# Optimization experiments

Hardware: AMD Instinct MI355X
Metric: run time of the kernel (lower is better)

The kernel has to match this reference:

```python
import jax, jax.numpy as jnp
import numpy as np

B, T, N, M = 128, 128, 32, 128  # batch, window(input_len), driving_series, hidden_size


def _lstm_cell(x_t, h, c, Wih, Whh, bih, bhh):
    # PyTorch gate order: i, f, g, o
    g = x_t @ Wih.T + bih + h @ Whh.T + bhh
    i, f, gg, o = jnp.split(g, 4, axis=-1)
    c = jax.nn.sigmoid(f) * c + jax.nn.sigmoid(i) * jnp.tanh(gg)
    h = jax.nn.sigmoid(o) * jnp.tanh(c)
    return h, c


def _lstm_seq(x, Wih, Whh, bih, bhh):
    # x: [B,T,n] -> outputs [B,T,m], zero init state
    Bc = x.shape[0]
    m = Whh.shape[1]
    def step(carry, x_t):
        h, c = carry
        h, c = _lstm_cell(x_t, h, c, Wih, Whh, bih, bhh)
        return (h, c), h
    h0 = jnp.zeros((Bc, m), x.dtype)
    (_, _), ys = jax.lax.scan(step, (h0, h0), jnp.swapaxes(x, 0, 1))
    return jnp.swapaxes(ys, 0, 1)


def _forward(x, Wih0, Whh0, bih0, bhh0, We, Ue, Ve,
             Wg, bg, Wa, ba,
             Wih1, Whh1, bih1, bhh1, Wih2, Whh2, bih2, bhh2):
    Bc, Tc, n = x.shape
    m = Whh0.shape[1]
    ux = jnp.einsum('btn,mn->btm', x, Ue)  # Ue(x), constant across steps

    def step(carry, x_t):
        h, c = carry
        hs = jnp.concatenate([h, c], axis=-1)              # [B,2m]
        e = jnp.tanh(ux + (hs @ We.T)[:, None, :]) @ Ve[0]  # [B,T]
        a = jax.nn.softmax(e, axis=1)
        ia_t = jnp.einsum('bt,btn->bn', a, x)              # attended input at step t
        h, c = _lstm_cell(x_t, h, c, Wih0, Whh0, bih0, bhh0)
        return (h, c), ia_t

    h0 = jnp.zeros((Bc, m), x.dtype)
    (_, _), ia = jax.lax.scan(step, (h0, h0), jnp.swapaxes(x, 0, 1))
    input_attention = jnp.swapaxes(ia, 0, 1)               # [B,T,n]

    # self (spatial) attention, fully vectorized over t
    g = jnp.tanh(jnp.einsum('btn,mn->btm', x, Wg) + bg)
    a = jax.nn.sigmoid(jnp.einsum('btm,nm->btn', g, Wa) + ba)
    self_attention = a * x                                  # [B,T,n]

    out1 = _lstm_seq(input_attention, Wih1, Whh1, bih1, bhh1)
    out2 = _lstm_seq(self_attention, Wih2, Whh2, bih2, bhh2)
    return jnp.concatenate([out1, out2], axis=-1)           # [B,T,2m]


def setup_inputs() -> dict:
    key = jax.random.key(0)
    ks = jax.random.split(key, 20)
    stdv = 1.0 / np.sqrt(M)
    u = lambda k, shp: jax.random.uniform(k, shp, jnp.float32, -stdv, stdv)
    inp = {
        'x': jax.random.normal(ks[0], (B, T, N), jnp.float32),
        'Wih0': u(ks[1], (4 * M, N)), 'Whh0': u(ks[2], (4 * M, M)),
        'bih0': u(ks[3], (4 * M,)), 'bhh0': u(ks[4], (4 * M,)),
        'We': u(ks[5], (M, 2 * M)), 'Ue': u(ks[6], (M, N)), 'Ve': u(ks[7], (1, M)),
        'Wg': u(ks[8], (M, N)), 'bg': u(ks[9], (M,)),
        'Wa': u(ks[10], (N, M)), 'ba': u(ks[11], (N,)),
        'Wih1': u(ks[12], (4 * M, N)), 'Whh1': u(ks[13], (4 * M, M)),
        'bih1': u(ks[14], (4 * M,)), 'bhh1': u(ks[15], (4 * M,)),
        'Wih2': u(ks[16], (4 * M, N)), 'Whh2': u(ks[17], (4 * M, M)),
        'bih2': u(ks[18], (4 * M,)), 'bhh2': u(ks[19], (4 * M,)),
    }
    return inp


def reference(x, Wih0, Whh0, bih0, bhh0, We, Ue, Ve, Wg, bg, Wa, ba,
              Wih1, Whh1, bih1, bhh1, Wih2, Whh2, bih2, bhh2):
    return _forward(x, Wih0, Whh0, bih0, bhh0, We, Ue, Ve, Wg, bg, Wa, ba,
                    Wih1, Whh1, bih1, bhh1, Wih2, Whh2, bih2, bhh2)
```

## Files before the change

### kernel.cpp

```cpp
#include <hip/hip_runtime.h>

#define DI __device__ __forceinline__

DI float fsig(float v)  { return 1.0f / (1.0f + __expf(-v)); }
DI float ftanh(float v) { return 1.0f - 2.0f / (__expf(2.0f * v) + 1.0f); }

template <int MODE>
DI void lstm_scan(const float* __restrict__ xin,
                  const float* __restrict__ Wih,
                  const float* __restrict__ Whh,
                  const float* __restrict__ bih,
                  const float* __restrict__ bhh,
                  float* __restrict__ rec,
                  float* __restrict__ outp,
                  float* lds)
{
    const int tid = threadIdx.x;
    float* xl  = lds;
    float* h   = lds + 4096;
    float* c   = lds + 4224;
    float* act = lds + 4352;

    for (int i = tid; i < 4096; i += 512) xl[i] = xin[i];
    if (tid < 128) { h[tid] = 0.f; c[tid] = 0.f; }

    float4 wi[8], wh[32];
    {
        const float4* p = (const float4*)(Wih + tid * 32);
        #pragma unroll
        for (int i = 0; i < 8; ++i) wi[i] = p[i];
        const float4* q2 = (const float4*)(Whh + tid * 128);
        #pragma unroll
        for (int i = 0; i < 32; ++i) wh[i] = q2[i];
    }
    const float bias = bih[tid] + bhh[tid];
    const int gate = tid >> 7;
    __syncthreads();

    for (int t = 0; t < 128; ++t) {
        if (MODE == 0) {
            if (tid < 256) rec[t * 256 + tid] = (tid < 128) ? h[tid] : c[tid - 128];
        }
        float acc = bias;
        const float4* x4 = (const float4*)(xl + t * 32);
        #pragma unroll
        for (int i = 0; i < 8; ++i) {
            float4 v = x4[i];
            acc += wi[i].x * v.x + wi[i].y * v.y + wi[i].z * v.z + wi[i].w * v.w;
        }
        const float4* h4 = (const float4*)h;
        #pragma unroll
        for (int i = 0; i < 32; ++i) {
            float4 v = h4[i];
            acc += wh[i].x * v.x + wh[i].y * v.y + wh[i].z * v.z + wh[i].w * v.w;
        }
        float a = (gate == 2) ? ftanh(acc) : fsig(acc);
        act[tid] = a;
        __syncthreads();
        if (tid < 128) {
            float iv = act[tid], fv = act[128 + tid], gv = act[256 + tid], ov = act[384 + tid];
            float cn = fv * c[tid] + iv * gv;
            float hn = ov * ftanh(cn);
            c[tid] = cn; h[tid] = hn;
            if (MODE == 1) outp[t * 256 + tid] = hn;
        }
        __syncthreads();
    }
}

DI void selfatt_body(const float* __restrict__ x, const float* __restrict__ Wg,
                     const float* __restrict__ bg, const float* __restrict__ Wa,
                     const float* __restrict__ ba, float* __restrict__ sa,
                     int b, float* s)
{
    float* xl  = s;
    float* Wgl = s + 4224;
    float* WaT = s + 8448;
    float* bgl = s + 12672;
    float* bal = s + 12800;
    float* gl  = s + 12832;
    float* pp  = s + 13344;

    const int tid = threadIdx.x;
    for (int i = tid; i < 4096; i += 512) {
        int r = i >> 5, n = i & 31;
        xl[r * 33 + n]  = x[b * 4096 + i];
        Wgl[r * 33 + n] = Wg[i];
        WaT[(i & 127) * 33 + (i >> 7)] = Wa[i];
    }
    if (tid < 128) bgl[tid] = bg[tid];
    else if (tid < 160) bal[tid - 128] = ba[tid - 128];
    __syncthreads();

    const int tl = tid >> 7;
    for (int it = 0; it < 32; ++it) {
        {   const int m = tid & 127;
            const int t = it * 4 + tl;
            float acc = bgl[m];
            #pragma unroll
            for (int n = 0; n < 32; ++n) acc += xl[t * 33 + n] * Wgl[m * 33 + n];
            gl[tl * 128 + m] = ftanh(acc);
        }
        __syncthreads();
        {   const int n = tid & 31, c = (tid >> 5) & 3;
            float acc = 0.f;
            #pragma unroll
            for (int j = 0; j < 32; ++j) {
                int m = c * 32 + j;
                acc += gl[tl * 128 + m] * WaT[m * 33 + n];
            }
            pp[(tl * 4 + c) * 32 + n] = acc;
        }
        __syncthreads();
        if (tid < 128) {
            const int tl2 = tid >> 5, n = tid & 31;
            const int t = it * 4 + tl2;
            float sv = pp[(tl2 * 4 + 0) * 32 + n] + pp[(tl2 * 4 + 1) * 32 + n]
                     + pp[(tl2 * 4 + 2) * 32 + n] + pp[(tl2 * 4 + 3) * 32 + n] + bal[n];
            sa[b * 4096 + t * 32 + n] = fsig(sv) * xl[t * 33 + n];
        }
        __syncthreads();
    }
}

__global__ __launch_bounds__(512)
void kA_lstm0_sa(const float* __restrict__ x,
                 const float* __restrict__ Wih0, const float* __restrict__ Whh0,
                 const float* __restrict__ bih0, const float* __restrict__ bhh0,
                 const float* __restrict__ Wg, const float* __restrict__ bg,
                 const float* __restrict__ Wa, const float* __restrict__ ba,
                 float* __restrict__ rec, float* __restrict__ sa)
{
    __shared__ float smem[13856];
    const int blk = blockIdx.x;
    if (blk < 128) {
        lstm_scan<0>(x + blk * 4096, Wih0, Whh0, bih0, bhh0,
                     rec + blk * 32768, nullptr, smem);
    } else {
        selfatt_body(x, Wg, bg, Wa, ba, sa, blk - 128, smem);
    }
}

__global__ __launch_bounds__(512)
void kC_lstm12(const float* __restrict__ ia, const float* __restrict__ sa,
               const float* __restrict__ Wih1, const float* __restrict__ Whh1,
               const float* __restrict__ bih1, const float* __restrict__ bhh1,
               const float* __restrict__ Wih2, const float* __restrict__ Whh2,
               const float* __restrict__ bih2, const float* __restrict__ bhh2,
               float* __restrict__ out)
{
    __shared__ float smem[4864];
    const int blk = blockIdx.x;
    if (blk < 128) {
        lstm_scan<1>(ia + blk * 4096, Wih1, Whh1, bih1, bhh1,
                     nullptr, out + blk * 32768, smem);
    } else {
        const int b = blk - 128;
        lstm_scan<1>(sa + b * 4096, Wih2, Whh2, bih2, bhh2,
                     nullptr, out + b * 32768 + 128, smem);
    }
}

__global__ __launch_bounds__(512, 4)
void kB_attn(const float* __restrict__ x,
             const float* __restrict__ Ue,
             const float* __restrict__ We,
             const float* __restrict__ Ve,
             const float* __restrict__ rec,
             float* __restrict__ ia)
{
    __shared__ float xl[4608];
    __shared__ float wl[4608];
    __shared__ float ubuf[4608];
    __shared__ float ev[128];
    __shared__ float av[128];
    __shared__ float iap[576];
    __shared__ float wred[2];
    __shared__ float wsum[2];

    const int tid = threadIdx.x;
    const int b  = blockIdx.x >> 2;
    const int tc = blockIdx.x & 3;
    const int ta = tid >> 2;
    const int q  = tid & 3;

    float4 wer[16];
    {
        const float4* p = (const float4*)(We + tid * 64);
        #pragma unroll
        for (int i = 0; i < 16; ++i) wer[i] = p[i];
    }
    for (int i = tid; i < 4096; i += 512)
        xl[(i >> 5) * 36 + (i & 31)] = x[b * 4096 + i];

    const long rbase = (long)b * 32768 + (long)tc * 32 * 256;
    for (int h2 = 0; h2 < 2; ++h2) {
        __syncthreads();
        #pragma unroll
        for (int s = 0; s < 8; ++s) {
            int f = tid + 512 * s;
            int tl = f >> 8, k = f & 255;
            ubuf[tl * 272 + (k >> 6) * 68 + (k & 63)] =
                rec[rbase + (h2 * 16 + tl) * 256 + k];
        }
        __syncthreads();
        for (int tl = 0; tl < 16; ++tl) {
            const float4* hp = (const float4*)(ubuf + tl * 272 + q * 68);
            float acc = 0.f;
            #pragma unroll
            for (int i = 0; i < 16; ++i) {
                float4 v = hp[i];
                acc += wer[i].x * v.x + wer[i].y * v.y + wer[i].z * v.z + wer[i].w * v.w;
            }
            acc += __shfl_xor(acc, 1);
            acc += __shfl_xor(acc, 2);
            if (q == 0)
                wl[(h2 * 16 + tl) * 144 + (ta & 3) * 36 + (ta >> 2)] = 2.0f * acc;
        }
    }
    __syncthreads();

    for (int i = tid; i < 4096; i += 512)
        ubuf[(i >> 5) * 36 + (i & 31)] = Ue[i];
    __syncthreads();

    float uxr[32];
    {
        float xr[32];
        const float4* xp = (const float4*)(xl + ta * 36);
        #pragma unroll
        for (int i = 0; i < 8; ++i) {
            float4 v = xp[i];
            xr[4*i] = v.x; xr[4*i+1] = v.y; xr[4*i+2] = v.z; xr[4*i+3] = v.w;
        }
        #pragma unroll
        for (int j = 0; j < 32; ++j) {
            const float4* up = (const float4*)(ubuf + (4 * j + q) * 36);
            float acc = 0.f;
            #pragma unroll
            for (int i = 0; i < 8; ++i) {
                float4 v = up[i];
                acc += xr[4*i] * v.x + xr[4*i+1] * v.y + xr[4*i+2] * v.z + xr[4*i+3] * v.w;
            }
            uxr[j] = 2.0f * acc;
        }
    }

    float ver[32];
    #pragma unroll
    for (int j = 0; j < 32; ++j) ver[j] = Ve[4 * j + q];
    float VeTot;
    {
        float vs = 0.f;
        #pragma unroll
        for (int j = 0; j < 32; ++j) vs += ver[j];
        vs += __shfl_xor(vs, 1);
        vs += __shfl_xor(vs, 2);
        VeTot = vs;
    }

    for (int tl = 0; tl < 32; ++tl) {
        const int t = tc * 32 + tl;
        float acc2 = 0.f;
        const float4* wr = (const float4*)(wl + tl * 144 + q * 36);
        #pragma unroll
        for (int j4 = 0; j4 < 8; ++j4) {
            float4 w4 = wr[j4];
            {   float zs = uxr[4*j4+0] + w4.x;
                acc2 += ver[4*j4+0] * __fdividef(2.0f, __expf(zs) + 1.0f); }
            {   float zs = uxr[4*j4+1] + w4.y;
                acc2 += ver[4*j4+1] * __fdividef(2.0f, __expf(zs) + 1.0f); }
            {   float zs = uxr[4*j4+2] + w4.z;
                acc2 += ver[4*j4+2] * __fdividef(2.0f, __expf(zs) + 1.0f); }
            {   float zs = uxr[4*j4+3] + w4.w;
                acc2 += ver[4*j4+3] * __fdividef(2.0f, __expf(zs) + 1.0f); }
        }
        acc2 += __shfl_xor(acc2, 1);
        acc2 += __shfl_xor(acc2, 2);
        if (q == 0) ev[ta] = VeTot - acc2;
        __syncthreads();

        float vv = 0.f, aa;
        if (tid < 128) {
            vv = ev[tid];
            float m2 = vv;
            #pragma unroll
            for (int o = 32; o > 0; o >>= 1) m2 = fmaxf(m2, __shfl_xor(m2, o));
            if ((tid & 63) == 0) wred[tid >> 6] = m2;
        }
        __syncthreads();
        if (tid < 128) {
            float M = fmaxf(wred[0], wred[1]);
            aa = __expf(vv - M);
            av[tid] = aa;
            float s = aa;
            #pragma unroll
            for (int o = 32; o > 0; o >>= 1) s += __shfl_xor(s, o);
            if ((tid & 63) == 0) wsum[tid >> 6] = s;
        }
        __syncthreads();
        {   const int n = tid & 31, g = tid >> 5;
            float accp = 0.f;
            #pragma unroll
            for (int jj = 0; jj < 8; ++jj) {
                const int t2 = g * 8 + jj;
                accp += av[t2] * xl[t2 * 36 + n];
            }
            iap[g * 36 + n] = accp;
        }
        __syncthreads();
        if (tid < 32) {
            float s = 0.f;
            #pragma unroll
            for (int g = 0; g < 16; ++g) s += iap[g * 36 + tid];
            float scale = __fdividef(1.0f, wsum[0] + wsum[1]);
            ia[((long)b * 128 + t) * 32 + tid] = s * scale;
        }
    }
}

extern "C" void kernel_launch(void* const* d_in, const int* in_sizes, int n_in,
                              void* d_out, int out_size, void* d_ws, size_t ws_size,
                              hipStream_t stream)
{
    const float* x    = (const float*)d_in[0];
    const float* Wih0 = (const float*)d_in[1];
    const float* Whh0 = (const float*)d_in[2];
    const float* bih0 = (const float*)d_in[3];
    const float* bhh0 = (const float*)d_in[4];
    const float* We   = (const float*)d_in[5];
    const float* Ue   = (const float*)d_in[6];
    const float* Ve   = (const float*)d_in[7];
    const float* Wg   = (const float*)d_in[8];
    const float* bg   = (const float*)d_in[9];
    const float* Wa   = (const float*)d_in[10];
    const float* ba   = (const float*)d_in[11];
    const float* Wih1 = (const float*)d_in[12];
    const float* Whh1 = (const float*)d_in[13];
    const float* bih1 = (const float*)d_in[14];
    const float* bhh1 = (const float*)d_in[15];
    const float* Wih2 = (const float*)d_in[16];
    const float* Whh2 = (const float*)d_in[17];
    const float* bih2 = (const float*)d_in[18];
    const float* bhh2 = (const float*)d_in[19];

    float* out = (float*)d_out;
    float* ws  = (float*)d_ws;
    float* sa  = ws;
    float* rec = ws + 524288;
    float* iaw = ws + 4718592;

    kA_lstm0_sa<<<256, 512, 0, stream>>>(x, Wih0, Whh0, bih0, bhh0,
                                         Wg, bg, Wa, ba, rec, sa);
    kB_attn<<<512, 512, 0, stream>>>(x, Ue, We, Ve, rec, iaw);
    kC_lstm12<<<256, 512, 0, stream>>>(iaw, sa, Wih1, Whh1, bih1, bhh1,
                                       Wih2, Whh2, bih2, bhh2, out);
}
```

Before: 528.9 us.

## Split LSTM gate matvec across K-quarters and keep cell state in registers

```diff
diff --git a/kernel.cpp b/kernel.cpp
--- a/kernel.cpp
+++ b/kernel.cpp
@@ -6,63 +6,106 @@
 DI float ftanh(float v) { return 1.0f - 2.0f / (__expf(2.0f * v) + 1.0f); }
 
 template <int MODE>
-DI void lstm_scan(const float* __restrict__ xin,
-                  const float* __restrict__ Wih,
-                  const float* __restrict__ Whh,
-                  const float* __restrict__ bih,
-                  const float* __restrict__ bhh,
-                  float* __restrict__ rec,
-                  float* __restrict__ outp,
-                  float* lds)
+DI void lstm_scan2(const float* __restrict__ xin,
+                   const float* __restrict__ Wih,
+                   const float* __restrict__ Whh,
+                   const float* __restrict__ bih,
+                   const float* __restrict__ bhh,
+                   float* __restrict__ rec,
+                   float* __restrict__ outp,
+                   float* lds)
 {
     const int tid = threadIdx.x;
-    float* xl  = lds;
-    float* h   = lds + 4096;
-    float* c   = lds + 4224;
-    float* act = lds + 4352;
+    const int r0 = tid & 127;
+    const int kq = tid >> 7;
+    float* xl = lds;
+    float* hl = lds + 4096;
+    float* pl = lds + 4224;
 
     for (int i = tid; i < 4096; i += 512) xl[i] = xin[i];
-    if (tid < 128) { h[tid] = 0.f; c[tid] = 0.f; }
-
-    float4 wi[8], wh[32];
-    {
-        const float4* p = (const float4*)(Wih + tid * 32);
-        #pragma unroll
-        for (int i = 0; i < 8; ++i) wi[i] = p[i];
-        const float4* q2 = (const float4*)(Whh + tid * 128);
-        #pragma unroll
-        for (int i = 0; i < 32; ++i) wh[i] = q2[i];
-    }
-    const float bias = bih[tid] + bhh[tid];
-    const int gate = tid >> 7;
+    if (tid < 128) hl[tid] = 0.f;
+
+    float4 wq[4][10];
+    if (kq == 0) {
+        #pragma unroll
+        for (int g = 0; g < 4; ++g) {
+            const int r = g * 128 + r0;
+            const float4* pi4 = (const float4*)(Wih + r * 32);
+            #pragma unroll
+            for (int i = 0; i < 8; ++i) wq[g][i] = pi4[i];
+            const float4* ph4 = (const float4*)(Whh + r * 128);
+            wq[g][8] = ph4[0]; wq[g][9] = ph4[1];
+        }
+    } else {
+        const int off = 40 * kq - 32;
+        #pragma unroll
+        for (int g = 0; g < 4; ++g) {
+            const int r = g * 128 + r0;
+            const float4* ph4 = (const float4*)(Whh + r * 128 + off);
+            #pragma unroll
+            for (int j = 0; j < 10; ++j) wq[g][j] = ph4[j];
+        }
+    }
+    float b0 = 0.f, b1 = 0.f, b2 = 0.f, b3 = 0.f, hreg = 0.f, creg = 0.f;
+    if (tid < 128) {
+        b0 = bih[tid]       + bhh[tid];
+        b1 = bih[128 + tid] + bhh[128 + tid];
+        b2 = bih[256 + tid] + bhh[256 + tid];
+        b3 = bih[384 + tid] + bhh[384 + tid];
+    }
     __syncthreads();
 
     for (int t = 0; t < 128; ++t) {
-        if (MODE == 0) {
-            if (tid < 256) rec[t * 256 + tid] = (tid < 128) ? h[tid] : c[tid - 128];
-        }
-        float acc = bias;
-        const float4* x4 = (const float4*)(xl + t * 32);
-        #pragma unroll
-        for (int i = 0; i < 8; ++i) {
-            float4 v = x4[i];
-            acc += wi[i].x * v.x + wi[i].y * v.y + wi[i].z * v.z + wi[i].w * v.w;
-        }
-        const float4* h4 = (const float4*)h;
-        #pragma unroll
-        for (int i = 0; i < 32; ++i) {
-            float4 v = h4[i];
-            acc += wh[i].x * v.x + wh[i].y * v.y + wh[i].z * v.z + wh[i].w * v.w;
-        }
-        float a = (gate == 2) ? ftanh(acc) : fsig(acc);
-        act[tid] = a;
+        float a0 = 0.f, a1 = 0.f, a2 = 0.f, a3 = 0.f;
+        if (kq == 0) {
+            const float4* x4 = (const float4*)(xl + t * 32);
+            #pragma unroll
+            for (int i = 0; i < 8; ++i) {
+                float4 v = x4[i];
+                a0 += wq[0][i].x * v.x + wq[0][i].y * v.y + wq[0][i].z * v.z + wq[0][i].w * v.w;
+                a1 += wq[1][i].x * v.x + wq[1][i].y * v.y + wq[1][i].z * v.z + wq[1][i].w * v.w;
+                a2 += wq[2][i].x * v.x + wq[2][i].y * v.y + wq[2][i].z * v.z + wq[2][i].w * v.w;
+                a3 += wq[3][i].x * v.x + wq[3][i].y * v.y + wq[3][i].z * v.z + wq[3][i].w * v.w;
+            }
+            const float4* h4 = (const float4*)hl;
+            #pragma unroll
+            for (int j = 0; j < 2; ++j) {
+                float4 v = h4[j];
+                a0 += wq[0][8+j].x * v.x + wq[0][8+j].y * v.y + wq[0][8+j].z * v.z + wq[0][8+j].w * v.w;
+                a1 += wq[1][8+j].x * v.x + wq[1][8+j].y * v.y + wq[1][8+j].z * v.z + wq[1][8+j].w * v.w;
+                a2 += wq[2][8+j].x * v.x + wq[2][8+j].y * v.y + wq[2][8+j].z * v.z + wq[2][8+j].w * v.w;
+                a3 += wq[3][8+j].x * v.x + wq[3][8+j].y * v.y + wq[3][8+j].z * v.z + wq[3][8+j].w * v.w;
+            }
+        } else {
+            const float4* h4 = (const float4*)(hl + 40 * kq - 32);
+            #pragma unroll
+            for (int j = 0; j < 10; ++j) {
+                float4 v = h4[j];
+                a0 += wq[0][j].x * v.x + wq[0][j].y * v.y + wq[0][j].z * v.z + wq[0][j].w * v.w;
+                a1 += wq[1][j].x * v.x + wq[1][j].y * v.y + wq[1][j].z * v.z + wq[1][j].w * v.w;
+                a2 += wq[2][j].x * v.x + wq[2][j].y * v.y + wq[2][j].z * v.z + wq[2][j].w * v.w;
+                a3 += wq[3][j].x * v.x + wq[3][j].y * v.y + wq[3][j].z * v.z + wq[3][j].w * v.w;
+            }
+        }
+        pl[kq * 512 +       r0] = a0;
+        pl[kq * 512 + 128 + r0] = a1;
+        pl[kq * 512 + 256 + r0] = a2;
+        pl[kq * 512 + 384 + r0] = a3;
         __syncthreads();
         if (tid < 128) {
-            float iv = act[tid], fv = act[128 + tid], gv = act[256 + tid], ov = act[384 + tid];
-            float cn = fv * c[tid] + iv * gv;
-            float hn = ov * ftanh(cn);
-            c[tid] = cn; h[tid] = hn;
-            if (MODE == 1) outp[t * 256 + tid] = hn;
+            float pi = b0 + pl[tid]        + pl[512 + tid]  + pl[1024 + tid] + pl[1536 + tid];
+            float pf = b1 + pl[128 + tid]  + pl[640 + tid]  + pl[1152 + tid] + pl[1664 + tid];
+            float pg = b2 + pl[256 + tid]  + pl[768 + tid]  + pl[1280 + tid] + pl[1792 + tid];
+            float po = b3 + pl[384 + tid]  + pl[896 + tid]  + pl[1408 + tid] + pl[1920 + tid];
+            if (MODE == 0) {
+                rec[t * 256 + tid]       = hreg;
+                rec[t * 256 + 128 + tid] = creg;
+            }
+            float iv = fsig(pi), fv = fsig(pf), gv = ftanh(pg), ov = fsig(po);
+            creg = fv * creg + iv * gv;
+            hreg = ov * ftanh(creg);
+            hl[tid] = hreg;
+            if (MODE == 1) outp[t * 256 + tid] = hreg;
         }
         __syncthreads();
     }
@@ -123,8 +166,8 @@
     }
 }
 
-__global__ __launch_bounds__(512)
-void kA_lstm0_sa(const float* __restrict__ x,
+__global__ __launch_bounds__(512, 2)
+void k1_lstm0_sa(const float* __restrict__ x,
                  const float* __restrict__ Wih0, const float* __restrict__ Whh0,
                  const float* __restrict__ bih0, const float* __restrict__ bhh0,
                  const float* __restrict__ Wg, const float* __restrict__ bg,
@@ -134,30 +177,30 @@
     __shared__ float smem[13856];
     const int blk = blockIdx.x;
     if (blk < 128) {
-        lstm_scan<0>(x + blk * 4096, Wih0, Whh0, bih0, bhh0,
-                     rec + blk * 32768, nullptr, smem);
+        lstm_scan2<0>(x + blk * 4096, Wih0, Whh0, bih0, bhh0,
+                      rec + blk * 32768, nullptr, smem);
     } else {
         selfatt_body(x, Wg, bg, Wa, ba, sa, blk - 128, smem);
     }
 }
 
-__global__ __launch_bounds__(512)
-void kC_lstm12(const float* __restrict__ ia, const float* __restrict__ sa,
+__global__ __launch_bounds__(512, 2)
+void k3_lstm12(const float* __restrict__ ia, const float* __restrict__ sa,
                const float* __restrict__ Wih1, const float* __restrict__ Whh1,
                const float* __restrict__ bih1, const float* __restrict__ bhh1,
                const float* __restrict__ Wih2, const float* __restrict__ Whh2,
                const float* __restrict__ bih2, const float* __restrict__ bhh2,
                float* __restrict__ out)
 {
-    __shared__ float smem[4864];
+    __shared__ float smem[6272];
     const int blk = blockIdx.x;
     if (blk < 128) {
-        lstm_scan<1>(ia + blk * 4096, Wih1, Whh1, bih1, bhh1,
-                     nullptr, out + blk * 32768, smem);
+        lstm_scan2<1>(ia + blk * 4096, Wih1, Whh1, bih1, bhh1,
+                      nullptr, out + blk * 32768, smem);
     } else {
         const int b = blk - 128;
-        lstm_scan<1>(sa + b * 4096, Wih2, Whh2, bih2, bhh2,
-                     nullptr, out + b * 32768 + 128, smem);
+        lstm_scan2<1>(sa + b * 4096, Wih2, Whh2, bih2, bhh2,
+                      nullptr, out + b * 32768 + 128, smem);
     }
 }
 
@@ -246,17 +289,22 @@
         }
     }
 
-    float ver[32];
+    float ver2[32];
     #pragma unroll
-    for (int j = 0; j < 32; ++j) ver[j] = Ve[4 * j + q];
+    for (int j = 0; j < 32; ++j) ver2[j] = 2.0f * Ve[4 * j + q];
     float VeTot;
     {
         float vs = 0.f;
         #pragma unroll
-        for (int j = 0; j < 32; ++j) vs += ver[j];
+        for (int j = 0; j < 32; ++j) vs += ver2[j];
         vs += __shfl_xor(vs, 1);
         vs += __shfl_xor(vs, 2);
-        VeTot = vs;
+        VeTot = 0.5f * vs;
+    }
+    #pragma unroll
+    for (int j = 0; j < 32; ++j) {
+        asm volatile("" : "+v"(uxr[j]));
+        asm volatile("" : "+v"(ver2[j]));
     }
 
     for (int tl = 0; tl < 32; ++tl) {
@@ -267,13 +315,13 @@
         for (int j4 = 0; j4 < 8; ++j4) {
             float4 w4 = wr[j4];
             {   float zs = uxr[4*j4+0] + w4.x;
-                acc2 += ver[4*j4+0] * __fdividef(2.0f, __expf(zs) + 1.0f); }
+                acc2 += ver2[4*j4+0] * __frcp_rn(__expf(zs) + 1.0f); }
             {   float zs = uxr[4*j4+1] + w4.y;
-                acc2 += ver[4*j4+1] * __fdividef(2.0f, __expf(zs) + 1.0f); }
+                acc2 += ver2[4*j4+1] * __frcp_rn(__expf(zs) + 1.0f); }
             {   float zs = uxr[4*j4+2] + w4.z;
-                acc2 += ver[4*j4+2] * __fdividef(2.0f, __expf(zs) + 1.0f); }
+                acc2 += ver2[4*j4+2] * __frcp_rn(__expf(zs) + 1.0f); }
             {   float zs = uxr[4*j4+3] + w4.w;
-                acc2 += ver[4*j4+3] * __fdividef(2.0f, __expf(zs) + 1.0f); }
+                acc2 += ver2[4*j4+3] * __frcp_rn(__expf(zs) + 1.0f); }
         }
         acc2 += __shfl_xor(acc2, 1);
         acc2 += __shfl_xor(acc2, 2);
@@ -350,9 +398,9 @@
     float* rec = ws + 524288;
     float* iaw = ws + 4718592;
 
-    kA_lstm0_sa<<<256, 512, 0, stream>>>(x, Wih0, Whh0, bih0, bhh0,
+    k1_lstm0_sa<<<256, 512, 0, stream>>>(x, Wih0, Whh0, bih0, bhh0,
                                          Wg, bg, Wa, ba, rec, sa);
     kB_attn<<<512, 512, 0, stream>>>(x, Ue, We, Ve, rec, iaw);
-    kC_lstm12<<<256, 512, 0, stream>>>(iaw, sa, Wih1, Whh1, bih1, bhh1,
+    k3_lstm12<<<256, 512, 0, stream>>>(iaw, sa, Wih1, Whh1, bih1, bhh1,
                                        Wih2, Whh2, bih2, bhh2, out);
 }
```

After: 568.4 us. 7.5% more time.
